# Performance work log

Measured on AMD Instinct MI355X. Metric: run time of the kernel, lower is better.

## Reference

```python
import jax, jax.numpy as jnp
import numpy as np


def _conv2d(x, w, stride, padding):
    # x: NCHW, w: OIHW
    return jax.lax.conv_general_dilated(
        x, w, window_strides=(stride, stride),
        padding=((padding, padding), (padding, padding)),
        dimension_numbers=('NCHW', 'OIHW', 'NCHW'))


def setup_inputs() -> dict:
    key = jax.random.key(0)
    k1, k2 = jax.random.split(key)
    B, C_in, H, Wd = 8, 64, 256, 256
    C_out, ksz = 64, 3
    x = jax.random.normal(k1, (B, C_in, H, Wd), dtype=jnp.float32)
    W = jax.random.normal(k2, (C_out, C_in, ksz, ksz), dtype=jnp.float32)
    b = jnp.zeros((C_out,), dtype=jnp.float32)
    return {"x": x, "W": W, "b": b}


def reference(x, W, b):
    stride, padding = 1, 1
    B, C, H, Wd = x.shape
    # per-pixel (across-channel) normalization of activations
    xf = jnp.transpose(x, (0, 2, 3, 1)).reshape(-1, C)       # [B*H*W, C]
    mu = jnp.mean(xf, axis=-1, keepdims=True)
    var = jnp.mean((xf - mu) ** 2, axis=-1, keepdims=True)    # unbiased=False
    r = 1.0 / jnp.sqrt(var + 1e-8)
    y_norm = r * (xf - mu)
    # int8 fake-quant per pixel
    s_act = 127.0 / jnp.maximum(jnp.max(jnp.abs(y_norm), axis=-1, keepdims=True), 1e-8)
    y_tilde = jnp.clip(jnp.round(s_act * y_norm), -128.0, 127.0) / s_act
    y4 = jnp.transpose(y_tilde.reshape(B, H, Wd, C), (0, 3, 1, 2))
    # ternary weight quant (value; STE only matters for backward)
    s_w = 1.0 / jnp.maximum(jnp.mean(jnp.abs(W)), 1e-8)
    w_tilde = jnp.clip(jnp.round(s_w * W), -1.0, 1.0) / s_w
    out = _conv2d(y4, w_tilde, stride, padding) + b[None, :, None, None]
    return out
```

## Files before the change

### kernel.cpp

```cpp
#include <hip/hip_runtime.h>
#include <hip/hip_bf16.h>

typedef _Float16 half8 __attribute__((ext_vector_type(8)));
typedef float    f32x4 __attribute__((ext_vector_type(4)));

#define NB   8
#define NC   64
#define NH   256
#define NW   256
#define NO   64
#define Y_OFF    0ull
#define Y_BYTES  (33554432ull * 2ull)
#define TW_OFF   (Y_OFF + Y_BYTES)
#define TW_BYTES (576ull * 64ull * 2ull)
#define MSW_OFF  (TW_OFF + TW_BYTES)

__global__ __launch_bounds__(256) void wq_kernel(const float* __restrict__ W,
                                                 _Float16* __restrict__ tw2,
                                                 float* __restrict__ msw_out) {
    __shared__ float red[256];
    __shared__ float sw_sh;
    int tid = threadIdx.x;
    float s = 0.0f;
    #pragma unroll
    for (int i = 0; i < 144; ++i) s += fabsf(W[i * 256 + tid]);
    red[tid] = s;
    __syncthreads();
    for (int off = 128; off > 0; off >>= 1) {
        if (tid < off) red[tid] += red[tid + off];
        __syncthreads();
    }
    if (tid == 0) {
        float mean = red[0] / 36864.0f;
        float msw  = fmaxf(mean, 1e-8f);
        sw_sh      = 1.0f / msw;
        msw_out[0] = msw;
    }
    __syncthreads();
    float s_w = sw_sh;
    #pragma unroll
    for (int i = 0; i < 144; ++i) {
        int idx = i * 256 + tid;
        float t = rintf(s_w * W[idx]);
        t = fminf(1.0f, fmaxf(-1.0f, t));
        int o  = idx / 576;
        int r  = idx - o * 576;
        int c  = r / 9;
        int r2 = r - c * 9;
        int kh = r2 / 3;
        int kw = r2 - kh * 3;
        int k  = (kh * 3 + kw) * 64 + c;
        tw2[((k >> 3) * 64 + o) * 8 + (k & 7)] = (_Float16)t;
    }
}

__global__ __launch_bounds__(256, 2) void norm_kernel(const float* __restrict__ x,
                                                      _Float16* __restrict__ y) {
    int p  = blockIdx.x * 256 + threadIdx.x;
    int bb = p >> 16;
    int hw = p & 65535;
    const float* xp = x + (size_t)bb * 64 * 65536 + hw;

    float v[64];
    float s = 0.0f;
    #pragma unroll
    for (int c = 0; c < 64; ++c) { v[c] = xp[(size_t)c * 65536]; s += v[c]; }
    float mu = s * (1.0f / 64.0f);

    float var = 0.0f, dmax = 0.0f;
    #pragma unroll
    for (int c = 0; c < 64; ++c) {
        float d = v[c] - mu;
        var += d * d;
        dmax = fmaxf(dmax, fabsf(d));
    }
    var *= (1.0f / 64.0f);
    float r    = 1.0f / sqrtf(var + 1e-8f);
    float amax = fmaxf(dmax * r, 1e-8f);
    float s_a  = 127.0f / amax;
    float invs = amax / 127.0f;

    half8 hv[8];
    #pragma unroll
    for (int c = 0; c < 64; ++c) {
        float yn = (v[c] - mu) * r;
        float q  = rintf(s_a * yn);
        q = fminf(127.0f, fmaxf(-128.0f, q));
        hv[c >> 3][c & 7] = (_Float16)(q * invs);
    }
    half8* yp = (half8*)(y + (size_t)p * 64);
    #pragma unroll
    for (int j = 0; j < 8; ++j) yp[j] = hv[j];
}

__global__ __launch_bounds__(256, 2) void conv_kernel(const _Float16* __restrict__ y,
                                                      const _Float16* __restrict__ tw2,
                                                      const float* __restrict__ msw_p,
                                                      const float* __restrict__ bias,
                                                      float* __restrict__ out) {
    __shared__ alignas(16) _Float16 lds[3 * 8 * 66 * 8];

    int tid = threadIdx.x;
    int bid = blockIdx.x;
    int wt = bid & 3;
    int h  = (bid >> 2) & 255;
    int bb = bid >> 10;
    int w0 = wt * 64;

    for (int i = tid; i < 1584; i += 256) {
        int cc = i & 7;
        int t8 = i >> 3;
        int wl = t8 % 66;
        int kh = t8 / 66;
        int hp = h + kh - 1;
        int wp = w0 + wl - 1;
        half8 val;
        #pragma unroll
        for (int e = 0; e < 8; ++e) val[e] = (_Float16)0.0f;
        if ((unsigned)hp < 256u && (unsigned)wp < 256u)
            val = *(const half8*)(y + ((((size_t)bb * 256 + hp) * 256 + wp) * 64 + cc * 8));
        *(half8*)(lds + ((kh * 8 + cc) * 66 + wl) * 8) = val;
    }

    int l   = tid & 63;
    int wv  = tid >> 6;
    int l15 = l & 15;
    int q8  = l >> 4;

    half8 aw[18];
    #pragma unroll
    for (int ks = 0; ks < 18; ++ks)
        aw[ks] = *(const half8*)(tw2 + (((ks * 4 + q8) * 64) + wv * 16 + l15) * 8);

    __syncthreads();

    f32x4 acc[4];
    #pragma unroll
    for (int nt = 0; nt < 4; ++nt)
        #pragma unroll
        for (int r2 = 0; r2 < 4; ++r2) acc[nt][r2] = 0.0f;

    #pragma unroll
    for (int ks = 0; ks < 18; ++ks) {
        int tap = ks >> 1;
        int kh  = tap / 3;
        int kw  = tap - kh * 3;
        int ccb = (ks & 1) * 4 + q8;
        int base = ((kh * 8 + ccb) * 66 + kw + l15) * 8;
        #pragma unroll
        for (int nt = 0; nt < 4; ++nt) {
            half8 bf = *(const half8*)(lds + base + nt * 128);
            acc[nt] = __builtin_amdgcn_mfma_f32_16x16x32_f16(aw[ks], bf, acc[nt], 0, 0, 0);
        }
    }

    float msw = *msw_p;
    size_t obase = ((size_t)bb * 64) * 65536 + (size_t)h * 256;
    #pragma unroll
    for (int reg = 0; reg < 4; ++reg) {
        int o = wv * 16 + q8 * 4 + reg;
        float bo = bias[o];
        #pragma unroll
        for (int nt = 0; nt < 4; ++nt) {
            int w = w0 + nt * 16 + l15;
            out[obase + (size_t)o * 65536 + w] = acc[nt][reg] * msw + bo;
        }
    }
}

extern "C" void kernel_launch(void* const* d_in, const int* in_sizes, int n_in,
                              void* d_out, int out_size, void* d_ws, size_t ws_size,
                              hipStream_t stream) {
    const float* x = (const float*)d_in[0];
    const float* W = (const float*)d_in[1];
    const float* b = (const float*)d_in[2];
    float* out = (float*)d_out;

    char* ws = (char*)d_ws;
    _Float16* y   = (_Float16*)(ws + Y_OFF);
    _Float16* tw2 = (_Float16*)(ws + TW_OFF);
    float*    msw = (float*)(ws + MSW_OFF);

    wq_kernel<<<1, 256, 0, stream>>>(W, tw2, msw);
    norm_kernel<<<2048, 256, 0, stream>>>(x, y);
    conv_kernel<<<8192, 256, 0, stream>>>(y, tw2, msw, b, out);
}
```

Measured before the change: 314.6 us.

## Fuse per-pixel normalization and fake-quant into the conv kernel

Removes the separate normalization kernel and its fp16 intermediate buffer. Each conv block now reads raw fp32 input for its 3x66 halo pixels, normalizes and quantizes them per pixel, and writes the result straight into LDS. This drops the 64 MB intermediate write and read, but the 3-row halo means each input pixel is normalized about three times and read from fp32 three times, which may partly hit in cache. Block IDs are remapped so neighbouring rows run close together for cache reuse, and the occupancy hint is raised to 3.

Measured after the change: 330.0 us. +4.9%, slower.

```diff
diff --git a/kernel.cpp b/kernel.cpp
--- a/kernel.cpp
+++ b/kernel.cpp
@@ -1,5 +1,4 @@
 #include <hip/hip_runtime.h>
-#include <hip/hip_bf16.h>
 
 typedef _Float16 half8 __attribute__((ext_vector_type(8)));
 typedef float    f32x4 __attribute__((ext_vector_type(4)));
@@ -9,9 +8,7 @@
 #define NH   256
 #define NW   256
 #define NO   64
-#define Y_OFF    0ull
-#define Y_BYTES  (33554432ull * 2ull)
-#define TW_OFF   (Y_OFF + Y_BYTES)
+#define TW_OFF   0ull
 #define TW_BYTES (576ull * 64ull * 2ull)
 #define MSW_OFF  (TW_OFF + TW_BYTES)
 
@@ -54,72 +51,61 @@
     }
 }
 
-__global__ __launch_bounds__(256, 2) void norm_kernel(const float* __restrict__ x,
-                                                      _Float16* __restrict__ y) {
-    int p  = blockIdx.x * 256 + threadIdx.x;
-    int bb = p >> 16;
-    int hw = p & 65535;
-    const float* xp = x + (size_t)bb * 64 * 65536 + hw;
-
-    float v[64];
-    float s = 0.0f;
-    #pragma unroll
-    for (int c = 0; c < 64; ++c) { v[c] = xp[(size_t)c * 65536]; s += v[c]; }
-    float mu = s * (1.0f / 64.0f);
-
-    float var = 0.0f, dmax = 0.0f;
-    #pragma unroll
-    for (int c = 0; c < 64; ++c) {
-        float d = v[c] - mu;
-        var += d * d;
-        dmax = fmaxf(dmax, fabsf(d));
-    }
-    var *= (1.0f / 64.0f);
-    float r    = 1.0f / sqrtf(var + 1e-8f);
-    float amax = fmaxf(dmax * r, 1e-8f);
-    float s_a  = 127.0f / amax;
-    float invs = amax / 127.0f;
-
-    half8 hv[8];
-    #pragma unroll
-    for (int c = 0; c < 64; ++c) {
-        float yn = (v[c] - mu) * r;
-        float q  = rintf(s_a * yn);
-        q = fminf(127.0f, fmaxf(-128.0f, q));
-        hv[c >> 3][c & 7] = (_Float16)(q * invs);
-    }
-    half8* yp = (half8*)(y + (size_t)p * 64);
-    #pragma unroll
-    for (int j = 0; j < 8; ++j) yp[j] = hv[j];
-}
-
-__global__ __launch_bounds__(256, 2) void conv_kernel(const _Float16* __restrict__ y,
-                                                      const _Float16* __restrict__ tw2,
-                                                      const float* __restrict__ msw_p,
-                                                      const float* __restrict__ bias,
-                                                      float* __restrict__ out) {
+__global__ __launch_bounds__(256, 3) void fused_kernel(const float* __restrict__ x,
+                                                       const _Float16* __restrict__ tw2,
+                                                       const float* __restrict__ msw_p,
+                                                       const float* __restrict__ bias,
+                                                       float* __restrict__ out) {
     __shared__ alignas(16) _Float16 lds[3 * 8 * 66 * 8];
 
     int tid = threadIdx.x;
-    int bid = blockIdx.x;
+    int pb  = blockIdx.x;
+    int bid = (pb & 7) * 1024 + (pb >> 3);
     int wt = bid & 3;
     int h  = (bid >> 2) & 255;
     int bb = bid >> 10;
     int w0 = wt * 64;
 
-    for (int i = tid; i < 1584; i += 256) {
-        int cc = i & 7;
-        int t8 = i >> 3;
-        int wl = t8 % 66;
-        int kh = t8 / 66;
+    if (tid < 198) {
+        int kh = tid / 66;
+        int wl = tid - kh * 66;
         int hp = h + kh - 1;
         int wp = w0 + wl - 1;
-        half8 val;
+        float v[64];
+        float s = 0.0f;
+        if ((unsigned)hp < 256u && (unsigned)wp < 256u) {
+            const float* xp = x + (size_t)bb * 64 * 65536 + (size_t)hp * 256 + wp;
+            #pragma unroll
+            for (int c = 0; c < 64; ++c) { v[c] = xp[(size_t)c * 65536]; s += v[c]; }
+        } else {
+            #pragma unroll
+            for (int c = 0; c < 64; ++c) v[c] = 0.0f;
+        }
+        float mu = s * (1.0f / 64.0f);
+        float var = 0.0f, dmax = 0.0f;
         #pragma unroll
-        for (int e = 0; e < 8; ++e) val[e] = (_Float16)0.0f;
-        if ((unsigned)hp < 256u && (unsigned)wp < 256u)
-            val = *(const half8*)(y + ((((size_t)bb * 256 + hp) * 256 + wp) * 64 + cc * 8));
-        *(half8*)(lds + ((kh * 8 + cc) * 66 + wl) * 8) = val;
+        for (int c = 0; c < 64; ++c) {
+            float d = v[c] - mu;
+            var += d * d;
+            dmax = fmaxf(dmax, fabsf(d));
+        }
+        var *= (1.0f / 64.0f);
+        float r    = 1.0f / sqrtf(var + 1e-8f);
+        float amax = fmaxf(dmax * r, 1e-8f);
+        float s_a  = 127.0f / amax;
+        float invs = amax / 127.0f;
+        #pragma unroll
+        for (int cc = 0; cc < 8; ++cc) {
+            half8 hv;
+            #pragma unroll
+            for (int j = 0; j < 8; ++j) {
+                float yn = (v[cc * 8 + j] - mu) * r;
+                float q  = rintf(s_a * yn);
+                q = fminf(127.0f, fmaxf(-128.0f, q));
+                hv[j] = (_Float16)(q * invs);
+            }
+            *(half8*)(lds + ((kh * 8 + cc) * 66 + wl) * 8) = hv;
+        }
     }
 
     int l   = tid & 63;
@@ -177,11 +163,9 @@
     float* out = (float*)d_out;
 
     char* ws = (char*)d_ws;
-    _Float16* y   = (_Float16*)(ws + Y_OFF);
     _Float16* tw2 = (_Float16*)(ws + TW_OFF);
     float*    msw = (float*)(ws + MSW_OFF);
 
     wq_kernel<<<1, 256, 0, stream>>>(W, tw2, msw);
-    norm_kernel<<<2048, 256, 0, stream>>>(x, y);
-    conv_kernel<<<8192, 256, 0, stream>>>(y, tw2, msw, b, out);
+    fused_kernel<<<8192, 256, 0, stream>>>(x, tw2, msw, b, out);
 }
```
